# Optimization experiments

Hardware: AMD Instinct MI355X
Metric: run time of the kernel (lower is better)

The kernel has to match this reference:

```python
import jax, jax.numpy as jnp
import numpy as np

N_DRUG = 50000
N_GENE = 50000
E = 600000
D_IN = 128
D_HID = 64
D_EMB = 32


def setup_inputs() -> dict:
    key = jax.random.key(0)
    ks = jax.random.split(key, 32)
    inp = {}
    inp['x_drug'] = jax.random.normal(ks[0], (N_DRUG, D_IN), jnp.float32)
    inp['x_gene'] = jax.random.normal(ks[1], (N_GENE, D_IN), jnp.float32)
    # per-etype edge lists (src,dst)
    inp['dd_src'] = jax.random.randint(ks[2], (E,), 0, N_DRUG)
    inp['dd_dst'] = jax.random.randint(ks[3], (E,), 0, N_DRUG)
    inp['dg_src'] = jax.random.randint(ks[4], (E,), 0, N_DRUG)
    inp['dg_dst'] = jax.random.randint(ks[5], (E,), 0, N_GENE)
    inp['gd_src'] = jax.random.randint(ks[6], (E,), 0, N_GENE)
    inp['gd_dst'] = jax.random.randint(ks[7], (E,), 0, N_DRUG)
    inp['gg_src'] = jax.random.randint(ks[8], (E,), 0, N_GENE)
    inp['gg_dst'] = jax.random.randint(ks[9], (E,), 0, N_GENE)
    # layer-1 per-relation weights (in -> hidden) and per-ntype biases
    s1 = 1.0 / np.sqrt(D_IN)
    inp['W1_dd'] = jax.random.normal(ks[10], (D_IN, D_HID), jnp.float32) * s1
    inp['W1_dg'] = jax.random.normal(ks[11], (D_IN, D_HID), jnp.float32) * s1
    inp['W1_gd'] = jax.random.normal(ks[12], (D_IN, D_HID), jnp.float32) * s1
    inp['W1_gg'] = jax.random.normal(ks[13], (D_IN, D_HID), jnp.float32) * s1
    inp['b1_drug'] = jnp.zeros((D_HID,), jnp.float32)
    inp['b1_gene'] = jnp.zeros((D_HID,), jnp.float32)
    # layer-2 per-relation weights (hidden -> embed) and per-ntype biases
    s2 = 1.0 / np.sqrt(D_HID)
    inp['W2_dd'] = jax.random.normal(ks[14], (D_HID, D_EMB), jnp.float32) * s2
    inp['W2_dg'] = jax.random.normal(ks[15], (D_HID, D_EMB), jnp.float32) * s2
    inp['W2_gd'] = jax.random.normal(ks[16], (D_HID, D_EMB), jnp.float32) * s2
    inp['W2_gg'] = jax.random.normal(ks[17], (D_HID, D_EMB), jnp.float32) * s2
    inp['b2_drug'] = jnp.zeros((D_EMB,), jnp.float32)
    inp['b2_gene'] = jnp.zeros((D_EMB,), jnp.float32)
    return inp


def _rel_mean(x_src, W, src, dst, n_dst):
    # transform-then-gather (efficient when out_dim <= in_dim), segment-mean over dst
    m = (x_src @ W)[src]                                  # [E, out]
    s = jax.ops.segment_sum(m, dst, num_segments=n_dst)   # [n_dst, out]
    deg = jax.ops.segment_sum(jnp.ones((src.shape[0],), m.dtype), dst, num_segments=n_dst)
    return s / jnp.maximum(deg, 1.0)[:, None]


def _rgcn_layer(xd, xg, Wdd, Wdg, Wgd, Wgg, bd, bg,
                dd_src, dd_dst, dg_src, dg_dst, gd_src, gd_dst, gg_src, gg_dst, act):
    hd = (_rel_mean(xd, Wdd, dd_src, dd_dst, N_DRUG)
          + _rel_mean(xg, Wgd, gd_src, gd_dst, N_DRUG) + bd)
    hg = (_rel_mean(xd, Wdg, dg_src, dg_dst, N_GENE)
          + _rel_mean(xg, Wgg, gg_src, gg_dst, N_GENE) + bg)
    if act:
        hd = jax.nn.relu(hd)
        hg = jax.nn.relu(hg)
    return hd, hg


def reference(x_drug, x_gene, dd_src, dd_dst, dg_src, dg_dst, gd_src, gd_dst,
              gg_src, gg_dst, W1_dd, W1_dg, W1_gd, W1_gg, b1_drug, b1_gene,
              W2_dd, W2_dg, W2_gd, W2_gg, b2_drug, b2_gene):
    hd, hg = _rgcn_layer(x_drug, x_gene, W1_dd, W1_dg, W1_gd, W1_gg, b1_drug, b1_gene,
                         dd_src, dd_dst, dg_src, dg_dst, gd_src, gd_dst, gg_src, gg_dst, True)
    hd, hg = _rgcn_layer(hd, hg, W2_dd, W2_dg, W2_gd, W2_gg, b2_drug, b2_gene,
                         dd_src, dd_dst, dg_src, dg_dst, gd_src, gd_dst, gg_src, gg_dst, False)
    # concatenate per-ntype embeddings: rows [0:N_DRUG]=drug, [N_DRUG:]=gene
    return jnp.concatenate([hd, hg], axis=0)
```

## Files before the change

### kernel.cpp

```cpp
#include <hip/hip_runtime.h>
#include <hip/hip_bf16.h>

#define N_NODE 50000
#define NEDGE  600000
#define NRANGE 128
#define RSZ    391
#define CAPB   6144
#define CHUNK  4096
#define NBLK1  147
#define GEMM_GX 391

typedef __hip_bfloat16 bf16;
typedef __attribute__((ext_vector_type(8))) short short8;
typedef __attribute__((ext_vector_type(4))) float floatx4;

__device__ __forceinline__ short f2s(float f) {
    bf16 t = __float2bfloat16(f);
    return *(short*)&t;
}
__device__ __forceinline__ unsigned pk2(float lo, float hi) {
    return ((unsigned)(unsigned short)f2s(lo)) | (((unsigned)(unsigned short)f2s(hi)) << 16);
}
__device__ __forceinline__ void acc2(float& a, float& b, unsigned w, float m) {
    a += m * __uint_as_float(w << 16);
    b += m * __uint_as_float(w & 0xFFFF0000u);
}


__global__ __launch_bounds__(512) void k_part_gemm(
    const int* __restrict__ d0, const int* __restrict__ s0,
    const int* __restrict__ d1, const int* __restrict__ s1,
    const int* __restrict__ d2, const int* __restrict__ s2,
    const int* __restrict__ d3, const int* __restrict__ s3,
    int* __restrict__ gcur, unsigned* __restrict__ gpart,
    const float* __restrict__ X0, const float* __restrict__ X1,
    const float* __restrict__ Wa0, const float* __restrict__ Wb0,
    const float* __restrict__ Wa1, const float* __restrict__ Wb1,
    bf16* __restrict__ out0, bf16* __restrict__ out1)
{
    __shared__ union {
        struct { unsigned buf[CHUNK]; int sc[512]; int hcur[NRANGE]; int delta[NRANGE]; } p;
        short wl[4 * 8 * 512];
    } u;

    int tid = threadIdx.x;
    if (blockIdx.x < 4 * NBLK1) {
        int bid = blockIdx.x;
        int rel = bid / NBLK1;
        int c   = bid - rel * NBLK1;
        const int* dp = rel == 0 ? d0 : rel == 1 ? d1 : rel == 2 ? d2 : d3;
        const int* sp = rel == 0 ? s0 : rel == 1 ? s1 : rel == 2 ? s2 : s3;
        int e0 = c * CHUNK;
        int e1 = min(e0 + CHUNK, NEDGE);
        int cnt = e1 - e0;
        const int4* dp4 = (const int4*)(dp + e0);
        const int4* sp4 = (const int4*)(sp + e0);
        int nv = cnt >> 2;

        if (tid < NRANGE) u.p.hcur[tid] = 0;
        __syncthreads();
        for (int i = tid; i < nv; i += 512) {
            int4 d = dp4[i];
            atomicAdd(&u.p.hcur[d.x / RSZ], 1);
            atomicAdd(&u.p.hcur[d.y / RSZ], 1);
            atomicAdd(&u.p.hcur[d.z / RSZ], 1);
            atomicAdd(&u.p.hcur[d.w / RSZ], 1);
        }
        __syncthreads();
        int v = (tid < NRANGE) ? u.p.hcur[tid] : 0;
        u.p.sc[tid] = v;
        __syncthreads();
        for (int d = 1; d < NRANGE; d <<= 1) {
            int t = (tid >= d && tid < NRANGE) ? u.p.sc[tid - d] : 0;
            __syncthreads();
            if (tid < NRANGE) u.p.sc[tid] += t;
            __syncthreads();
        }
        if (tid < NRANGE) {
            int start = u.p.sc[tid] - v;
            int bg    = rel * NRANGE + tid;
            int resv  = atomicAdd(&gcur[bg], v);
            u.p.delta[tid] = bg * CAPB + resv - start;
            u.p.hcur[tid]  = start;
        }
        __syncthreads();
        for (int i = tid; i < nv; i += 512) {
            int4 d = dp4[i];
            int4 s = sp4[i];
#define PUT(dd, ss) { int b = (dd) / RSZ; int p = atomicAdd(&u.p.hcur[b], 1); \
                      u.p.buf[p] = ((unsigned)b << 25) | ((unsigned)((dd) - b * RSZ) << 16) | (unsigned)(ss); }
            PUT(d.x, s.x) PUT(d.y, s.y) PUT(d.z, s.z) PUT(d.w, s.w)
#undef PUT
        }
        __syncthreads();
        for (int i = tid * 4; i < cnt; i += 2048) {
            uint4 kb = *(const uint4*)&u.p.buf[i];
            gpart[u.p.delta[kb.x >> 25] + i + 0] = kb.x;
            gpart[u.p.delta[kb.y >> 25] + i + 1] = kb.y;
            gpart[u.p.delta[kb.z >> 25] + i + 2] = kb.z;
            gpart[u.p.delta[kb.w >> 25] + i + 3] = kb.w;
        }
    } else {
        constexpr int NB = 8, KC = 4, NH = 64;
        int bid2 = blockIdx.x - 4 * NBLK1;
        int sel  = bid2 >= GEMM_GX;
        int bx   = sel ? bid2 - GEMM_GX : bid2;
        const float* X  = sel ? X1 : X0;
        const float* Wa = sel ? Wa1 : Wa0;
        const float* Wb = sel ? Wb1 : Wb0;
        bf16*       outp = sel ? out1 : out0;

        for (int i = tid; i < KC * NB * 512; i += 512) {
            int j  = i & 7;
            int n  = (i >> 3) & 15;
            int q  = (i >> 7) & 3;
            int nb = (i >> 9) & (NB - 1);
            int kc = i >> 12;
            int k  = kc * 32 + q * 8 + j;
            int c  = nb * 16 + n;
            float w = (c < NH) ? Wa[k * NH + c] : Wb[k * NH + (c - NH)];
            u.wl[i] = f2s(w);
        }
        __syncthreads();

        int lane = tid & 63, wv = tid >> 6;
        int q = lane >> 4, lidx = lane & 15;
        int row0 = bx * 128 + wv * 16;
        int rowA = min(row0 + lidx, N_NODE - 1);

        floatx4 acc[NB];
#pragma unroll
        for (int nb = 0; nb < NB; nb++) acc[nb] = (floatx4){0.f, 0.f, 0.f, 0.f};

#pragma unroll
        for (int kc = 0; kc < KC; kc++) {
            const float* Xf = X + (size_t)rowA * 128 + kc * 32 + q * 8;
            float4 f0 = *(const float4*)Xf;
            float4 f1 = *(const float4*)(Xf + 4);
            short8 a;
            a[0] = f2s(f0.x); a[1] = f2s(f0.y); a[2] = f2s(f0.z); a[3] = f2s(f0.w);
            a[4] = f2s(f1.x); a[5] = f2s(f1.y); a[6] = f2s(f1.z); a[7] = f2s(f1.w);
#pragma unroll
            for (int nb = 0; nb < NB; nb++) {
                short8 b = *(const short8*)&u.wl[((kc * NB + nb) * 64 + lane) * 8];
                acc[nb] = __builtin_amdgcn_mfma_f32_16x16x32_bf16(a, b, acc[nb], 0, 0, 0);
            }
        }
#pragma unroll
        for (int nb = 0; nb < NB; nb++) {
#pragma unroll
            for (int r = 0; r < 4; r++) {
                int row = row0 + q * 4 + r;
                if (row < N_NODE)
                    outp[(size_t)row * 128 + nb * 16 + lidx] = __float2bfloat16(acc[nb][r]);
            }
        }
    }
}

__global__ __launch_bounds__(512) void k_csr(
    const unsigned* __restrict__ gpart, const int* __restrict__ gcnt,
    int* __restrict__ off, unsigned short* __restrict__ edges)
{
    __shared__ unsigned short stg[CAPB];
    __shared__ int cur[RSZ];
    __shared__ int sc[512];
    int bid = blockIdx.x;
    int rel = bid >> 7, r = bid & (NRANGE - 1);
    int tid = threadIdx.x;
    int range0 = r * RSZ;
    int RS = min(RSZ, N_NODE - range0);
    if (RS < 0) RS = 0;
    int count = gcnt[bid];
    const uint4* gp4 = (const uint4*)(gpart + (size_t)bid * CAPB);
    const unsigned* gp = gpart + (size_t)bid * CAPB;
    int count4 = count & ~3;

    int vb = (tid < NRANGE) ? gcnt[rel * NRANGE + tid] : 0;
    sc[tid] = vb;
    __syncthreads();
    for (int d = 1; d < NRANGE; d <<= 1) {
        int t = (tid >= d && tid < NRANGE) ? sc[tid - d] : 0;
        __syncthreads();
        if (tid < NRANGE) sc[tid] += t;
        __syncthreads();
    }
    int base = (r > 0) ? sc[r - 1] : 0;
    __syncthreads();

    for (int i = tid; i < RSZ; i += 512) cur[i] = 0;
    __syncthreads();
    for (int i = tid * 4; i < count4; i += 2048) {
        uint4 g = gp4[i >> 2];
        atomicAdd(&cur[(g.x >> 16) & 0x1FF], 1);
        atomicAdd(&cur[(g.y >> 16) & 0x1FF], 1);
        atomicAdd(&cur[(g.z >> 16) & 0x1FF], 1);
        atomicAdd(&cur[(g.w >> 16) & 0x1FF], 1);
    }
    if (tid < (count & 3))
        atomicAdd(&cur[(gp[count4 + tid] >> 16) & 0x1FF], 1);
    __syncthreads();
    int x = (tid < RSZ) ? cur[tid] : 0;
    sc[tid] = x;
    __syncthreads();
    for (int d = 1; d < 512; d <<= 1) {
        int t = (tid >= d) ? sc[tid - d] : 0;
        __syncthreads();
        sc[tid] += t;
        __syncthreads();
    }
    int excl = sc[tid] - x;
    __syncthreads();
    if (tid < RSZ) cur[tid] = excl;
    __syncthreads();
    for (int i = tid; i < RS; i += 512)
        off[rel * (N_NODE + 1) + range0 + i] = base + cur[i];
    if (r == NRANGE - 1 && tid == 0) off[rel * (N_NODE + 1) + N_NODE] = NEDGE;
    __syncthreads();
    for (int i = tid * 4; i < count4; i += 2048) {
        uint4 g = gp4[i >> 2];
#define SCAT(gg) { int p = atomicAdd(&cur[((gg) >> 16) & 0x1FF], 1); stg[p] = (unsigned short)((gg) & 0xFFFFu); }
        SCAT(g.x) SCAT(g.y) SCAT(g.z) SCAT(g.w)
#undef SCAT
    }
    if (tid < (count & 3)) {
        unsigned g = gp[count4 + tid];
        int p = atomicAdd(&cur[(g >> 16) & 0x1FF], 1);
        stg[p] = (unsigned short)(g & 0xFFFFu);
    }
    __syncthreads();
    for (int i = tid; i < count; i += 512)
        edges[(size_t)rel * NEDGE + base + i] = stg[i];
}

template <int K, int NOUT, bool AFP32>
__global__ __launch_bounds__(256) void k_gemm_pair(
    const void* __restrict__ X0, const void* __restrict__ X1,
    const float* __restrict__ Wa0, const float* __restrict__ Wb0,
    const float* __restrict__ Wa1, const float* __restrict__ Wb1,
    bf16* __restrict__ out0, bf16* __restrict__ out1, int M)
{
    constexpr int NB  = NOUT / 16;
    constexpr int KC  = K / 32;
    constexpr int NH  = NOUT / 2;
    constexpr int NBL = (NB == 8) ? 3 : 2;
    __shared__ short Wl[KC * NB * 512];

    int sel = blockIdx.y;
    const void*  X  = sel ? X1 : X0;
    const float* Wa = sel ? Wa1 : Wa0;
    const float* Wb = sel ? Wb1 : Wb0;
    bf16*        out = sel ? out1 : out0;

    int tid = threadIdx.x;
    for (int i = tid; i < KC * NB * 512; i += 256) {
        int j  = i & 7;
        int n  = (i >> 3) & 15;
        int q  = (i >> 7) & 3;
        int nb = (i >> 9) & (NB - 1);
        int kc = i >> (9 + NBL);
        int k  = kc * 32 + q * 8 + j;
        int c  = nb * 16 + n;
        float w = (c < NH) ? Wa[k * NH + c] : Wb[k * NH + (c - NH)];
        Wl[i] = f2s(w);
    }
    __syncthreads();

    int lane = tid & 63, wv = tid >> 6;
    int q = lane >> 4, lidx = lane & 15;
    int row0 = blockIdx.x * 64 + wv * 16;
    int rowA = min(row0 + lidx, M - 1);

    floatx4 acc[NB];
#pragma unroll
    for (int nb = 0; nb < NB; nb++) acc[nb] = (floatx4){0.f, 0.f, 0.f, 0.f};

#pragma unroll
    for (int kc = 0; kc < KC; kc++) {
        short8 a;
        if constexpr (AFP32) {
            const float* Xf = (const float*)X + (size_t)rowA * K + kc * 32 + q * 8;
            float4 f0 = *(const float4*)Xf;
            float4 f1 = *(const float4*)(Xf + 4);
            a[0] = f2s(f0.x); a[1] = f2s(f0.y); a[2] = f2s(f0.z); a[3] = f2s(f0.w);
            a[4] = f2s(f1.x); a[5] = f2s(f1.y); a[6] = f2s(f1.z); a[7] = f2s(f1.w);
        } else {
            a = *(const short8*)((const short*)X + (size_t)rowA * K + kc * 32 + q * 8);
        }
#pragma unroll
        for (int nb = 0; nb < NB; nb++) {
            short8 b = *(const short8*)&Wl[((kc * NB + nb) * 64 + lane) * 8];
            acc[nb] = __builtin_amdgcn_mfma_f32_16x16x32_bf16(a, b, acc[nb], 0, 0, 0);
        }
    }
#pragma unroll
    for (int nb = 0; nb < NB; nb++) {
#pragma unroll
        for (int r = 0; r < 4; r++) {
            int row = row0 + q * 4 + r;
            if (row < M)
                out[(size_t)row * NOUT + nb * 16 + lidx] = __float2bfloat16(acc[nb][r]);
        }
    }
}

template<int ROWU>
__device__ __forceinline__ void seg_run(
    int n, const unsigned short* __restrict__ ep, float sc,
    const unsigned* __restrict__ base, float* s)
{
    int nfull = n & ~3;
    for (int i = 0; i < nfull; i += 4) {
        int e0 = ep[i + 0];
        int e1 = ep[i + 1];
        int e2 = ep[i + 2];
        int e3 = ep[i + 3];
        uint4 w0 = *(const uint4*)(base + e0 * ROWU);
        uint4 w1 = *(const uint4*)(base + e1 * ROWU);
        uint4 w2 = *(const uint4*)(base + e2 * ROWU);
        uint4 w3 = *(const uint4*)(base + e3 * ROWU);
        acc2(s[0], s[1], w0.x, sc); acc2(s[2], s[3], w0.y, sc);
        acc2(s[4], s[5], w0.z, sc); acc2(s[6], s[7], w0.w, sc);
        acc2(s[0], s[1], w1.x, sc); acc2(s[2], s[3], w1.y, sc);
        acc2(s[4], s[5], w1.z, sc); acc2(s[6], s[7], w1.w, sc);
        acc2(s[0], s[1], w2.x, sc); acc2(s[2], s[3], w2.y, sc);
        acc2(s[4], s[5], w2.z, sc); acc2(s[6], s[7], w2.w, sc);
        acc2(s[0], s[1], w3.x, sc); acc2(s[2], s[3], w3.y, sc);
        acc2(s[4], s[5], w3.z, sc); acc2(s[6], s[7], w3.w, sc);
    }
    for (int i = nfull; i < n; i++) {
        int e = ep[i];
        uint4 w = *(const uint4*)(base + e * ROWU);
        acc2(s[0], s[1], w.x, sc); acc2(s[2], s[3], w.y, sc);
        acc2(s[4], s[5], w.z, sc); acc2(s[6], s[7], w.w, sc);
    }
}

__global__ __launch_bounds__(256) void k_gather64v5(
    const bf16* __restrict__ m1,
    const int* __restrict__ offA0, const unsigned short* __restrict__ eA0,
    const int* __restrict__ offB0, const unsigned short* __restrict__ eB0,
    const float* __restrict__ bias0, bf16* __restrict__ out0,
    const int* __restrict__ offA1, const unsigned short* __restrict__ eA1,
    const int* __restrict__ offB1, const unsigned short* __restrict__ eB1,
    const float* __restrict__ bias1, bf16* __restrict__ out1)
{
    int tid  = threadIdx.x;
    int gid  = blockIdx.x * 32 + (tid >> 3);
    int lidx = tid & 7;
    int half = (gid >= N_NODE);
    int wid  = gid - (half ? N_NODE : 0);
    const int* offA = half ? offA1 : offA0;
    const unsigned short* eA = half ? eA1 : eA0;
    const int* offB = half ? offB1 : offB0;
    const unsigned short* eB = half ? eB1 : eB0;
    const float* bias = half ? bias1 : bias0;
    bf16* out = half ? out1 : out0;

    const unsigned* base = (const unsigned*)m1 + (half ? 32 : 0) + lidx * 4;

    int begA = offA[wid], nA = offA[wid + 1] - begA;
    int begB = offB[wid], nB = offB[wid + 1] - begB;
    float ia = 1.f / (float)max(nA, 1);
    float ib = 1.f / (float)max(nB, 1);

    float s[8] = {0.f,0.f,0.f,0.f,0.f,0.f,0.f,0.f};
    seg_run<64>(nA, eA + begA, ia, base, s);
    seg_run<64>(nB, eB + begB, ib, base + N_NODE * 64, s);

    float h[8];
#pragma unroll
    for (int k = 0; k < 8; k++)
        h[k] = fmaxf(s[k] + bias[lidx * 8 + k], 0.f);
    uint4 v;
    v.x = pk2(h[0], h[1]); v.y = pk2(h[2], h[3]);
    v.z = pk2(h[4], h[5]); v.w = pk2(h[6], h[7]);
    *(uint4*)(out + (size_t)wid * 64 + lidx * 8) = v;
}

__global__ __launch_bounds__(256) void k_gather32v2(
    const bf16* __restrict__ m2,
    const int* __restrict__ offA0, const unsigned short* __restrict__ eA0,
    const int* __restrict__ offB0, const unsigned short* __restrict__ eB0,
    const float* __restrict__ bias0, float* __restrict__ out0,
    const int* __restrict__ offA1, const unsigned short* __restrict__ eA1,
    const int* __restrict__ offB1, const unsigned short* __restrict__ eB1,
    const float* __restrict__ bias1, float* __restrict__ out1)
{
    int tid  = threadIdx.x;
    int gid  = blockIdx.x * 64 + (tid >> 2);
    int lidx = tid & 3;
    if (gid >= 2 * N_NODE) return;
    int half = (gid >= N_NODE);
    int wid  = gid - (half ? N_NODE : 0);
    const int* offA = half ? offA1 : offA0;
    const unsigned short* eA = half ? eA1 : eA0;
    const int* offB = half ? offB1 : offB0;
    const unsigned short* eB = half ? eB1 : eB0;
    const float* bias = half ? bias1 : bias0;
    float* out = half ? out1 : out0;

    const unsigned* base = (const unsigned*)m2 + (half ? 16 : 0) + lidx * 4;

    int begA = offA[wid], nA = offA[wid + 1] - begA;
    int begB = offB[wid], nB = offB[wid + 1] - begB;
    float ia = 1.f / (float)max(nA, 1);
    float ib = 1.f / (float)max(nB, 1);

    float s[8] = {0.f,0.f,0.f,0.f,0.f,0.f,0.f,0.f};
    seg_run<32>(nA, eA + begA, ia, base, s);
    seg_run<32>(nB, eB + begB, ib, base + N_NODE * 32, s);

    float* o = out + (size_t)wid * 32 + lidx * 8;
    float4 v0, v1;
    v0.x = s[0] + bias[lidx * 8 + 0];
    v0.y = s[1] + bias[lidx * 8 + 1];
    v0.z = s[2] + bias[lidx * 8 + 2];
    v0.w = s[3] + bias[lidx * 8 + 3];
    v1.x = s[4] + bias[lidx * 8 + 4];
    v1.y = s[5] + bias[lidx * 8 + 5];
    v1.z = s[6] + bias[lidx * 8 + 6];
    v1.w = s[7] + bias[lidx * 8 + 7];
    *(float4*)o = v0;
    *(float4*)(o + 4) = v1;
}

extern "C" void kernel_launch(void* const* d_in, const int* in_sizes, int n_in,
                              void* d_out, int out_size, void* d_ws, size_t ws_size,
                              hipStream_t stream)
{
    const float* xd = (const float*)d_in[0];
    const float* xg = (const float*)d_in[1];
    const int* dd_src = (const int*)d_in[2];  const int* dd_dst = (const int*)d_in[3];
    const int* dg_src = (const int*)d_in[4];  const int* dg_dst = (const int*)d_in[5];
    const int* gd_src = (const int*)d_in[6];  const int* gd_dst = (const int*)d_in[7];
    const int* gg_src = (const int*)d_in[8];  const int* gg_dst = (const int*)d_in[9];
    const float* W1dd = (const float*)d_in[10];
    const float* W1dg = (const float*)d_in[11];
    const float* W1gd = (const float*)d_in[12];
    const float* W1gg = (const float*)d_in[13];
    const float* b1d  = (const float*)d_in[14];
    const float* b1g  = (const float*)d_in[15];
    const float* W2dd = (const float*)d_in[16];
    const float* W2dg = (const float*)d_in[17];
    const float* W2gd = (const float*)d_in[18];
    const float* W2gg = (const float*)d_in[19];
    const float* b2d  = (const float*)d_in[20];
    const float* b2g  = (const float*)d_in[21];
    float* out = (float*)d_out;

    int* gcur     = (int*)d_ws;
    int* off      = gcur + 512;
    unsigned short* edges = (unsigned short*)(off + 4 * (N_NODE + 1));
    bf16* md1     = (bf16*)(edges + (size_t)4 * NEDGE);
    bf16* mg1     = md1 + (size_t)N_NODE * 128;
    bf16* h       = mg1 + (size_t)N_NODE * 128;
    bf16* hd      = h;
    bf16* hg      = h + (size_t)N_NODE * 64;
    bf16* md2     = md1;
    bf16* mg2     = md1 + (size_t)N_NODE * 64;
    unsigned* gpart = (unsigned*)h;

    hipMemsetAsync(gcur, 0, 512 * sizeof(int), stream);
    k_part_gemm<<<4 * NBLK1 + 2 * GEMM_GX, 512, 0, stream>>>(
        dd_dst, dd_src, gd_dst, gd_src, dg_dst, dg_src, gg_dst, gg_src, gcur, gpart,
        xd, xg, W1dd, W1dg, W1gd, W1gg, md1, mg1);

    k_csr<<<512, 512, 0, stream>>>(gpart, gcur, off, edges);

    const int* off_dd = off + 0 * (N_NODE + 1);
    const int* off_gd = off + 1 * (N_NODE + 1);
    const int* off_dg = off + 2 * (N_NODE + 1);
    const int* off_gg = off + 3 * (N_NODE + 1);
    const unsigned short* e_dd = edges + (size_t)0 * NEDGE;
    const unsigned short* e_gd = edges + (size_t)1 * NEDGE;
    const unsigned short* e_dg = edges + (size_t)2 * NEDGE;
    const unsigned short* e_gg = edges + (size_t)3 * NEDGE;

    int g64_grid = (2 * N_NODE) / 32;
    int g32_grid = (2 * N_NODE + 63) / 64;
    dim3 gemm2_grid((N_NODE + 63) / 64, 2);

    k_gather64v5<<<g64_grid, 256, 0, stream>>>(
        md1,
        off_dd, e_dd, off_gd, e_gd, b1d, hd,
        off_dg, e_dg, off_gg, e_gg, b1g, hg);

    k_gemm_pair<64, 64, false><<<gemm2_grid, 256, 0, stream>>>(
        hd, hg, W2dd, W2dg, W2gd, W2gg, md2, mg2, N_NODE);

    k_gather32v2<<<g32_grid, 256, 0, stream>>>(
        md2,
        off_dd, e_dd, off_gd, e_gd, b2d, out,
        off_dg, e_dg, off_gg, e_gg, b2g, out + (size_t)N_NODE * 32);
}
```

Before: 295.9 us.

## Replace two-level partition CSR build with global histogram, offset scan, and atomic scatter

Edge-to-CSR construction no longer partitions packed keys into per-range buckets in shared memory and a global staging buffer. It now keeps per-node degree counts in global memory via atomics, computes offsets in a scan kernel, and scatters source ids with global atomics on per-node cursors. This removes the gpart staging round-trip and the local sort passes. In exchange it adds one kernel launch, a larger memset, and many contended global atomics. Edge order within each node is no longer deterministic, which can change float summation order.

```diff
diff --git a/kernel.cpp b/kernel.cpp
--- a/kernel.cpp
+++ b/kernel.cpp
@@ -2,10 +2,10 @@
 #include <hip/hip_bf16.h>
 
 #define N_NODE 50000
+#define NPAD   50048
 #define NEDGE  600000
 #define NRANGE 128
 #define RSZ    391
-#define CAPB   6144
 #define CHUNK  4096
 #define NBLK1  147
 #define GEMM_GX 391
@@ -27,19 +27,17 @@
 }
 
 
-__global__ __launch_bounds__(512) void k_part_gemm(
-    const int* __restrict__ d0, const int* __restrict__ s0,
-    const int* __restrict__ d1, const int* __restrict__ s1,
-    const int* __restrict__ d2, const int* __restrict__ s2,
-    const int* __restrict__ d3, const int* __restrict__ s3,
-    int* __restrict__ gcur, unsigned* __restrict__ gpart,
+__global__ __launch_bounds__(512) void k_hist_gemm(
+    const int* __restrict__ d0, const int* __restrict__ d1,
+    const int* __restrict__ d2, const int* __restrict__ d3,
+    int* __restrict__ rsum, int* __restrict__ cnt,
     const float* __restrict__ X0, const float* __restrict__ X1,
     const float* __restrict__ Wa0, const float* __restrict__ Wb0,
     const float* __restrict__ Wa1, const float* __restrict__ Wb1,
     bf16* __restrict__ out0, bf16* __restrict__ out1)
 {
     __shared__ union {
-        struct { unsigned buf[CHUNK]; int sc[512]; int hcur[NRANGE]; int delta[NRANGE]; } p;
+        int hcur[NRANGE];
         short wl[4 * 8 * 512];
     } u;
 
@@ -49,56 +47,25 @@
         int rel = bid / NBLK1;
         int c   = bid - rel * NBLK1;
         const int* dp = rel == 0 ? d0 : rel == 1 ? d1 : rel == 2 ? d2 : d3;
-        const int* sp = rel == 0 ? s0 : rel == 1 ? s1 : rel == 2 ? s2 : s3;
         int e0 = c * CHUNK;
         int e1 = min(e0 + CHUNK, NEDGE);
-        int cnt = e1 - e0;
+        int nv = (e1 - e0) >> 2;
         const int4* dp4 = (const int4*)(dp + e0);
-        const int4* sp4 = (const int4*)(sp + e0);
-        int nv = cnt >> 2;
-
-        if (tid < NRANGE) u.p.hcur[tid] = 0;
+        int* cntr = cnt + rel * NPAD;
+
+        if (tid < NRANGE) u.hcur[tid] = 0;
         __syncthreads();
         for (int i = tid; i < nv; i += 512) {
             int4 d = dp4[i];
-            atomicAdd(&u.p.hcur[d.x / RSZ], 1);
-            atomicAdd(&u.p.hcur[d.y / RSZ], 1);
-            atomicAdd(&u.p.hcur[d.z / RSZ], 1);
-            atomicAdd(&u.p.hcur[d.w / RSZ], 1);
-        }
-        __syncthreads();
-        int v = (tid < NRANGE) ? u.p.hcur[tid] : 0;
-        u.p.sc[tid] = v;
-        __syncthreads();
-        for (int d = 1; d < NRANGE; d <<= 1) {
-            int t = (tid >= d && tid < NRANGE) ? u.p.sc[tid - d] : 0;
-            __syncthreads();
-            if (tid < NRANGE) u.p.sc[tid] += t;
-            __syncthreads();
-        }
+            atomicAdd(&cntr[d.x], 1); atomicAdd(&u.hcur[d.x / RSZ], 1);
+            atomicAdd(&cntr[d.y], 1); atomicAdd(&u.hcur[d.y / RSZ], 1);
+            atomicAdd(&cntr[d.z], 1); atomicAdd(&u.hcur[d.z / RSZ], 1);
+            atomicAdd(&cntr[d.w], 1); atomicAdd(&u.hcur[d.w / RSZ], 1);
+        }
+        __syncthreads();
         if (tid < NRANGE) {
-            int start = u.p.sc[tid] - v;
-            int bg    = rel * NRANGE + tid;
-            int resv  = atomicAdd(&gcur[bg], v);
-            u.p.delta[tid] = bg * CAPB + resv - start;
-            u.p.hcur[tid]  = start;
-        }
-        __syncthreads();
-        for (int i = tid; i < nv; i += 512) {
-            int4 d = dp4[i];
-            int4 s = sp4[i];
-#define PUT(dd, ss) { int b = (dd) / RSZ; int p = atomicAdd(&u.p.hcur[b], 1); \
-                      u.p.buf[p] = ((unsigned)b << 25) | ((unsigned)((dd) - b * RSZ) << 16) | (unsigned)(ss); }
-            PUT(d.x, s.x) PUT(d.y, s.y) PUT(d.z, s.z) PUT(d.w, s.w)
-#undef PUT
-        }
-        __syncthreads();
-        for (int i = tid * 4; i < cnt; i += 2048) {
-            uint4 kb = *(const uint4*)&u.p.buf[i];
-            gpart[u.p.delta[kb.x >> 25] + i + 0] = kb.x;
-            gpart[u.p.delta[kb.y >> 25] + i + 1] = kb.y;
-            gpart[u.p.delta[kb.z >> 25] + i + 2] = kb.z;
-            gpart[u.p.delta[kb.w >> 25] + i + 3] = kb.w;
+            int v = u.hcur[tid];
+            if (v) atomicAdd(&rsum[rel * NRANGE + tid], v);
         }
     } else {
         constexpr int NB = 8, KC = 4, NH = 64;
@@ -158,25 +125,18 @@
     }
 }
 
-__global__ __launch_bounds__(512) void k_csr(
-    const unsigned* __restrict__ gpart, const int* __restrict__ gcnt,
-    int* __restrict__ off, unsigned short* __restrict__ edges)
-{
-    __shared__ unsigned short stg[CAPB];
-    __shared__ int cur[RSZ];
+__global__ __launch_bounds__(512) void k_off(
+    const int* __restrict__ rsum, const int* __restrict__ cnt,
+    int* __restrict__ off, int* __restrict__ cur)
+{
     __shared__ int sc[512];
     int bid = blockIdx.x;
     int rel = bid >> 7, r = bid & (NRANGE - 1);
     int tid = threadIdx.x;
     int range0 = r * RSZ;
     int RS = min(RSZ, N_NODE - range0);
-    if (RS < 0) RS = 0;
-    int count = gcnt[bid];
-    const uint4* gp4 = (const uint4*)(gpart + (size_t)bid * CAPB);
-    const unsigned* gp = gpart + (size_t)bid * CAPB;
-    int count4 = count & ~3;
-
-    int vb = (tid < NRANGE) ? gcnt[rel * NRANGE + tid] : 0;
+
+    int vb = (tid < NRANGE) ? rsum[rel * NRANGE + tid] : 0;
     sc[tid] = vb;
     __syncthreads();
     for (int d = 1; d < NRANGE; d <<= 1) {
@@ -185,22 +145,10 @@
         if (tid < NRANGE) sc[tid] += t;
         __syncthreads();
     }
-    int base = (r > 0) ? sc[r - 1] : 0;
+    int rbase = (r > 0) ? sc[r - 1] : 0;
     __syncthreads();
 
-    for (int i = tid; i < RSZ; i += 512) cur[i] = 0;
-    __syncthreads();
-    for (int i = tid * 4; i < count4; i += 2048) {
-        uint4 g = gp4[i >> 2];
-        atomicAdd(&cur[(g.x >> 16) & 0x1FF], 1);
-        atomicAdd(&cur[(g.y >> 16) & 0x1FF], 1);
-        atomicAdd(&cur[(g.z >> 16) & 0x1FF], 1);
-        atomicAdd(&cur[(g.w >> 16) & 0x1FF], 1);
-    }
-    if (tid < (count & 3))
-        atomicAdd(&cur[(gp[count4 + tid] >> 16) & 0x1FF], 1);
-    __syncthreads();
-    int x = (tid < RSZ) ? cur[tid] : 0;
+    int x = (tid < RSZ) ? cnt[rel * NPAD + range0 + tid] : 0;
     sc[tid] = x;
     __syncthreads();
     for (int d = 1; d < 512; d <<= 1) {
@@ -209,28 +157,40 @@
         sc[tid] += t;
         __syncthreads();
     }
-    int excl = sc[tid] - x;
-    __syncthreads();
-    if (tid < RSZ) cur[tid] = excl;
-    __syncthreads();
-    for (int i = tid; i < RS; i += 512)
-        off[rel * (N_NODE + 1) + range0 + i] = base + cur[i];
+    int excl = rbase + sc[tid] - x;
+    if (tid < RSZ) cur[rel * NPAD + range0 + tid] = excl;
+    if (tid < RS)  off[rel * (N_NODE + 1) + range0 + tid] = excl;
     if (r == NRANGE - 1 && tid == 0) off[rel * (N_NODE + 1) + N_NODE] = NEDGE;
-    __syncthreads();
-    for (int i = tid * 4; i < count4; i += 2048) {
-        uint4 g = gp4[i >> 2];
-#define SCAT(gg) { int p = atomicAdd(&cur[((gg) >> 16) & 0x1FF], 1); stg[p] = (unsigned short)((gg) & 0xFFFFu); }
-        SCAT(g.x) SCAT(g.y) SCAT(g.z) SCAT(g.w)
-#undef SCAT
-    }
-    if (tid < (count & 3)) {
-        unsigned g = gp[count4 + tid];
-        int p = atomicAdd(&cur[(g >> 16) & 0x1FF], 1);
-        stg[p] = (unsigned short)(g & 0xFFFFu);
-    }
-    __syncthreads();
-    for (int i = tid; i < count; i += 512)
-        edges[(size_t)rel * NEDGE + base + i] = stg[i];
+}
+
+__global__ __launch_bounds__(512) void k_scatter(
+    const int* __restrict__ d0, const int* __restrict__ s0,
+    const int* __restrict__ d1, const int* __restrict__ s1,
+    const int* __restrict__ d2, const int* __restrict__ s2,
+    const int* __restrict__ d3, const int* __restrict__ s3,
+    int* __restrict__ cur, unsigned short* __restrict__ edges)
+{
+    int bid = blockIdx.x;
+    int rel = bid / NBLK1;
+    int c   = bid - rel * NBLK1;
+    const int* dp = rel == 0 ? d0 : rel == 1 ? d1 : rel == 2 ? d2 : d3;
+    const int* sp = rel == 0 ? s0 : rel == 1 ? s1 : rel == 2 ? s2 : s3;
+    int e0 = c * CHUNK;
+    int e1 = min(e0 + CHUNK, NEDGE);
+    int nv = (e1 - e0) >> 2;
+    const int4* dp4 = (const int4*)(dp + e0);
+    const int4* sp4 = (const int4*)(sp + e0);
+    int* curr = cur + rel * NPAD;
+    unsigned short* er = edges + (size_t)rel * NEDGE;
+
+    for (int i = threadIdx.x; i < nv; i += 512) {
+        int4 d = dp4[i];
+        int4 s = sp4[i];
+        int p0 = atomicAdd(&curr[d.x], 1); er[p0] = (unsigned short)s.x;
+        int p1 = atomicAdd(&curr[d.y], 1); er[p1] = (unsigned short)s.y;
+        int p2 = atomicAdd(&curr[d.z], 1); er[p2] = (unsigned short)s.z;
+        int p3 = atomicAdd(&curr[d.w], 1); er[p3] = (unsigned short)s.w;
+    }
 }
 
 template <int K, int NOUT, bool AFP32>
@@ -449,24 +409,29 @@
     const float* b2g  = (const float*)d_in[21];
     float* out = (float*)d_out;
 
-    int* gcur     = (int*)d_ws;
-    int* off      = gcur + 512;
+    int* rsum = (int*)d_ws;
+    int* cnt  = rsum + 512;
+    int* cur  = cnt + 4 * NPAD;
+    int* off  = cur + 4 * NPAD;
     unsigned short* edges = (unsigned short*)(off + 4 * (N_NODE + 1));
-    bf16* md1     = (bf16*)(edges + (size_t)4 * NEDGE);
-    bf16* mg1     = md1 + (size_t)N_NODE * 128;
-    bf16* h       = mg1 + (size_t)N_NODE * 128;
-    bf16* hd      = h;
-    bf16* hg      = h + (size_t)N_NODE * 64;
-    bf16* md2     = md1;
-    bf16* mg2     = md1 + (size_t)N_NODE * 64;
-    unsigned* gpart = (unsigned*)h;
-
-    hipMemsetAsync(gcur, 0, 512 * sizeof(int), stream);
-    k_part_gemm<<<4 * NBLK1 + 2 * GEMM_GX, 512, 0, stream>>>(
-        dd_dst, dd_src, gd_dst, gd_src, dg_dst, dg_src, gg_dst, gg_src, gcur, gpart,
+    bf16* md1 = (bf16*)(edges + (size_t)4 * NEDGE);
+    bf16* mg1 = md1 + (size_t)N_NODE * 128;
+    bf16* h   = mg1 + (size_t)N_NODE * 128;
+    bf16* hd  = h;
+    bf16* hg  = h + (size_t)N_NODE * 64;
+    bf16* md2 = md1;
+    bf16* mg2 = md1 + (size_t)N_NODE * 64;
+
+    hipMemsetAsync(rsum, 0, (512 + 4 * NPAD) * sizeof(int), stream);
+
+    k_hist_gemm<<<4 * NBLK1 + 2 * GEMM_GX, 512, 0, stream>>>(
+        dd_dst, gd_dst, dg_dst, gg_dst, rsum, cnt,
         xd, xg, W1dd, W1dg, W1gd, W1gg, md1, mg1);
 
-    k_csr<<<512, 512, 0, stream>>>(gpart, gcur, off, edges);
+    k_off<<<512, 512, 0, stream>>>(rsum, cnt, off, cur);
+
+    k_scatter<<<4 * NBLK1, 512, 0, stream>>>(
+        dd_dst, dd_src, gd_dst, gd_src, dg_dst, dg_src, gg_dst, gg_src, cur, edges);
 
     const int* off_dd = off + 0 * (N_NODE + 1);
     const int* off_gd = off + 1 * (N_NODE + 1);
```

After: 533.3 us. 1.8x slower.

## Fuse layer-2 GEMM into layer-1 gather kernel via LDS-staged hidden tile

Applied to the files above, without the earlier changes.

The layer-1 gather kernel now keeps its 32-row hidden tile in shared memory and immediately multiplies it by the layer-2 weights with MFMA, writing the layer-2 messages directly. This removes the separate GEMM launch and the global round trip of the hidden activations. In exchange, every gather block reloads and converts all four layer-2 weight matrices into LDS and adds a barrier, which raises per-block overhead and LDS use.

```diff
diff --git a/kernel.cpp b/kernel.cpp
--- a/kernel.cpp
+++ b/kernel.cpp
@@ -231,77 +231,6 @@
     __syncthreads();
     for (int i = tid; i < count; i += 512)
         edges[(size_t)rel * NEDGE + base + i] = stg[i];
-}
-
-template <int K, int NOUT, bool AFP32>
-__global__ __launch_bounds__(256) void k_gemm_pair(
-    const void* __restrict__ X0, const void* __restrict__ X1,
-    const float* __restrict__ Wa0, const float* __restrict__ Wb0,
-    const float* __restrict__ Wa1, const float* __restrict__ Wb1,
-    bf16* __restrict__ out0, bf16* __restrict__ out1, int M)
-{
-    constexpr int NB  = NOUT / 16;
-    constexpr int KC  = K / 32;
-    constexpr int NH  = NOUT / 2;
-    constexpr int NBL = (NB == 8) ? 3 : 2;
-    __shared__ short Wl[KC * NB * 512];
-
-    int sel = blockIdx.y;
-    const void*  X  = sel ? X1 : X0;
-    const float* Wa = sel ? Wa1 : Wa0;
-    const float* Wb = sel ? Wb1 : Wb0;
-    bf16*        out = sel ? out1 : out0;
-
-    int tid = threadIdx.x;
-    for (int i = tid; i < KC * NB * 512; i += 256) {
-        int j  = i & 7;
-        int n  = (i >> 3) & 15;
-        int q  = (i >> 7) & 3;
-        int nb = (i >> 9) & (NB - 1);
-        int kc = i >> (9 + NBL);
-        int k  = kc * 32 + q * 8 + j;
-        int c  = nb * 16 + n;
-        float w = (c < NH) ? Wa[k * NH + c] : Wb[k * NH + (c - NH)];
-        Wl[i] = f2s(w);
-    }
-    __syncthreads();
-
-    int lane = tid & 63, wv = tid >> 6;
-    int q = lane >> 4, lidx = lane & 15;
-    int row0 = blockIdx.x * 64 + wv * 16;
-    int rowA = min(row0 + lidx, M - 1);
-
-    floatx4 acc[NB];
-#pragma unroll
-    for (int nb = 0; nb < NB; nb++) acc[nb] = (floatx4){0.f, 0.f, 0.f, 0.f};
-
-#pragma unroll
-    for (int kc = 0; kc < KC; kc++) {
-        short8 a;
-        if constexpr (AFP32) {
-            const float* Xf = (const float*)X + (size_t)rowA * K + kc * 32 + q * 8;
-            float4 f0 = *(const float4*)Xf;
-            float4 f1 = *(const float4*)(Xf + 4);
-            a[0] = f2s(f0.x); a[1] = f2s(f0.y); a[2] = f2s(f0.z); a[3] = f2s(f0.w);
-            a[4] = f2s(f1.x); a[5] = f2s(f1.y); a[6] = f2s(f1.z); a[7] = f2s(f1.w);
-        } else {
-            a = *(const short8*)((const short*)X + (size_t)rowA * K + kc * 32 + q * 8);
-        }
-#pragma unroll
-        for (int nb = 0; nb < NB; nb++) {
-            short8 b = *(const short8*)&Wl[((kc * NB + nb) * 64 + lane) * 8];
-            acc[nb] = __builtin_amdgcn_mfma_f32_16x16x32_bf16(a, b, acc[nb], 0, 0, 0);
-        }
-    }
-#pragma unroll
-    for (int nb = 0; nb < NB; nb++) {
-#pragma unroll
-        for (int r = 0; r < 4; r++) {
-            int row = row0 + q * 4 + r;
-            if (row < M)
-                out[(size_t)row * NOUT + nb * 16 + lidx] = __float2bfloat16(acc[nb][r]);
-        }
-    }
 }
 
 template<int ROWU>
@@ -336,16 +265,38 @@
     }
 }
 
-__global__ __launch_bounds__(256) void k_gather64v5(
+__global__ __launch_bounds__(256) void k_gather64v6(
     const bf16* __restrict__ m1,
     const int* __restrict__ offA0, const unsigned short* __restrict__ eA0,
     const int* __restrict__ offB0, const unsigned short* __restrict__ eB0,
-    const float* __restrict__ bias0, bf16* __restrict__ out0,
+    const float* __restrict__ bias0,
     const int* __restrict__ offA1, const unsigned short* __restrict__ eA1,
     const int* __restrict__ offB1, const unsigned short* __restrict__ eB1,
-    const float* __restrict__ bias1, bf16* __restrict__ out1)
-{
+    const float* __restrict__ bias1,
+    const float* __restrict__ W2dd, const float* __restrict__ W2dg,
+    const float* __restrict__ W2gd, const float* __restrict__ W2gg,
+    bf16* __restrict__ m2)
+{
+    __shared__ short wd[4096];
+    __shared__ short wg[4096];
+    __shared__ short hlds[32 * 64];
+
     int tid  = threadIdx.x;
+
+    for (int i = tid; i < 4096; i += 256) {
+        int j  = i & 7;
+        int n  = (i >> 3) & 15;
+        int q  = (i >> 7) & 3;
+        int nb = (i >> 9) & 3;
+        int kc = i >> 11;
+        int k  = kc * 32 + q * 8 + j;
+        int c  = nb * 16 + n;
+        float w0 = (c < 32) ? W2dd[k * 32 + c] : W2dg[k * 32 + (c - 32)];
+        float w1 = (c < 32) ? W2gd[k * 32 + c] : W2gg[k * 32 + (c - 32)];
+        wd[i] = f2s(w0);
+        wg[i] = f2s(w1);
+    }
+
     int gid  = blockIdx.x * 32 + (tid >> 3);
     int lidx = tid & 7;
     int half = (gid >= N_NODE);
@@ -355,7 +306,6 @@
     const int* offB = half ? offB1 : offB0;
     const unsigned short* eB = half ? eB1 : eB0;
     const float* bias = half ? bias1 : bias0;
-    bf16* out = half ? out1 : out0;
 
     const unsigned* base = (const unsigned*)m1 + (half ? 32 : 0) + lidx * 4;
 
@@ -375,7 +325,33 @@
     uint4 v;
     v.x = pk2(h[0], h[1]); v.y = pk2(h[2], h[3]);
     v.z = pk2(h[4], h[5]); v.w = pk2(h[6], h[7]);
-    *(uint4*)(out + (size_t)wid * 64 + lidx * 8) = v;
+    *(uint4*)&hlds[(tid >> 3) * 64 + lidx * 8] = v;
+    __syncthreads();
+
+    int wv = tid >> 6, lane = tid & 63;
+    int q = lane >> 4, l16 = lane & 15;
+    int rt = wv >> 1;
+    int hrow = (blockIdx.x * 32 + rt * 16) >= N_NODE;
+    const short* wsel = hrow ? wg : wd;
+    int nb0 = (wv & 1) * 2, nb1 = nb0 + 1;
+
+    floatx4 acc0 = (floatx4){0.f,0.f,0.f,0.f};
+    floatx4 acc1 = (floatx4){0.f,0.f,0.f,0.f};
+#pragma unroll
+    for (int kc = 0; kc < 2; kc++) {
+        short8 a  = *(const short8*)&hlds[(rt * 16 + l16) * 64 + kc * 32 + q * 8];
+        short8 b0 = *(const short8*)&wsel[((kc * 4 + nb0) * 64 + lane) * 8];
+        short8 b1 = *(const short8*)&wsel[((kc * 4 + nb1) * 64 + lane) * 8];
+        acc0 = __builtin_amdgcn_mfma_f32_16x16x32_bf16(a, b0, acc0, 0, 0, 0);
+        acc1 = __builtin_amdgcn_mfma_f32_16x16x32_bf16(a, b1, acc1, 0, 0, 0);
+    }
+#pragma unroll
+    for (int r = 0; r < 4; r++) {
+        int row = rt * 16 + q * 4 + r;
+        bf16* o = m2 + ((size_t)blockIdx.x * 32 + row) * 64;
+        o[nb0 * 16 + l16] = __float2bfloat16(acc0[r]);
+        o[nb1 * 16 + l16] = __float2bfloat16(acc1[r]);
+    }
 }
 
 __global__ __launch_bounds__(256) void k_gather32v2(
@@ -454,12 +430,8 @@
     unsigned short* edges = (unsigned short*)(off + 4 * (N_NODE + 1));
     bf16* md1     = (bf16*)(edges + (size_t)4 * NEDGE);
     bf16* mg1     = md1 + (size_t)N_NODE * 128;
-    bf16* h       = mg1 + (size_t)N_NODE * 128;
-    bf16* hd      = h;
-    bf16* hg      = h + (size_t)N_NODE * 64;
-    bf16* md2     = md1;
-    bf16* mg2     = md1 + (size_t)N_NODE * 64;
-    unsigned* gpart = (unsigned*)h;
+    bf16* m2      = mg1 + (size_t)N_NODE * 128;
+    unsigned* gpart = (unsigned*)m2;
 
     hipMemsetAsync(gcur, 0, 512 * sizeof(int), stream);
     k_part_gemm<<<4 * NBLK1 + 2 * GEMM_GX, 512, 0, stream>>>(
@@ -479,18 +451,15 @@
 
     int g64_grid = (2 * N_NODE) / 32;
     int g32_grid = (2 * N_NODE + 63) / 64;
-    dim3 gemm2_grid((N_NODE + 63) / 64, 2);
-
-    k_gather64v5<<<g64_grid, 256, 0, stream>>>(
+
+    k_gather64v6<<<g64_grid, 256, 0, stream>>>(
         md1,
-        off_dd, e_dd, off_gd, e_gd, b1d, hd,
-        off_dg, e_dg, off_gg, e_gg, b1g, hg);
-
-    k_gemm_pair<64, 64, false><<<gemm2_grid, 256, 0, stream>>>(
-        hd, hg, W2dd, W2dg, W2gd, W2gg, md2, mg2, N_NODE);
+        off_dd, e_dd, off_gd, e_gd, b1d,
+        off_dg, e_dg, off_gg, e_gg, b1g,
+        W2dd, W2dg, W2gd, W2gg, m2);
 
     k_gather32v2<<<g32_grid, 256, 0, stream>>>(
-        md2,
+        m2,
         off_dd, e_dd, off_gd, e_gd, b2d, out,
         off_dg, e_dg, off_gg, e_gg, b2g, out + (size_t)N_NODE * 32);
 }
```

After: 297.9 us. Within noise of the previous version (+0.7%).

## Replace shared-memory block scans with wavefront shuffle scans; coarsen partition and GEMM blocks

Applied to the files above, without the earlier changes.

Replaces the barrier-heavy shared-memory Hillis-Steele scans in the partition and CSR kernels with wave-level shuffle scans plus a small cross-wave combine. This removes many __syncthreads calls. The CSR base offset becomes a shuffle reduction over the preceding ranges. Partition chunks double to 8192 edges, which halves the block count, and each GEMM block now processes two 128-row tiles so the LDS weight staging is amortised. The trade-off is fewer blocks and more LDS per partition block, which may lower occupancy and parallelism.

```diff
diff --git a/kernel.cpp b/kernel.cpp
--- a/kernel.cpp
+++ b/kernel.cpp
@@ -6,9 +6,9 @@
 #define NRANGE 128
 #define RSZ    391
 #define CAPB   6144
-#define CHUNK  4096
-#define NBLK1  147
-#define GEMM_GX 391
+#define CHUNK  8192
+#define NBLK1  74
+#define GEMM_GB 196
 
 typedef __hip_bfloat16 bf16;
 typedef __attribute__((ext_vector_type(8))) short short8;
@@ -24,6 +24,14 @@
 __device__ __forceinline__ void acc2(float& a, float& b, unsigned w, float m) {
     a += m * __uint_as_float(w << 16);
     b += m * __uint_as_float(w & 0xFFFF0000u);
+}
+__device__ __forceinline__ int wscan(int x, int lane) {
+#pragma unroll
+    for (int d = 1; d < 64; d <<= 1) {
+        int t = __shfl_up(x, d);
+        if (lane >= d) x += t;
+    }
+    return x;
 }
 
 
@@ -39,7 +47,7 @@
     bf16* __restrict__ out0, bf16* __restrict__ out1)
 {
     __shared__ union {
-        struct { unsigned buf[CHUNK]; int sc[512]; int hcur[NRANGE]; int delta[NRANGE]; } p;
+        struct { unsigned buf[CHUNK]; int hcur[NRANGE]; int delta[NRANGE]; int wsum[2]; } p;
         short wl[4 * 8 * 512];
     } u;
 
@@ -67,17 +75,14 @@
             atomicAdd(&u.p.hcur[d.w / RSZ], 1);
         }
         __syncthreads();
+        int lane = tid & 63, wv6 = tid >> 6;
         int v = (tid < NRANGE) ? u.p.hcur[tid] : 0;
-        u.p.sc[tid] = v;
+        int inc = wscan(v, lane);
+        if (lane == 63 && wv6 < 2) u.p.wsum[wv6] = inc;
         __syncthreads();
-        for (int d = 1; d < NRANGE; d <<= 1) {
-            int t = (tid >= d && tid < NRANGE) ? u.p.sc[tid - d] : 0;
-            __syncthreads();
-            if (tid < NRANGE) u.p.sc[tid] += t;
-            __syncthreads();
-        }
         if (tid < NRANGE) {
-            int start = u.p.sc[tid] - v;
+            int incl  = inc + ((wv6 == 1) ? u.p.wsum[0] : 0);
+            int start = incl - v;
             int bg    = rel * NRANGE + tid;
             int resv  = atomicAdd(&gcur[bg], v);
             u.p.delta[tid] = bg * CAPB + resv - start;
@@ -103,8 +108,8 @@
     } else {
         constexpr int NB = 8, KC = 4, NH = 64;
         int bid2 = blockIdx.x - 4 * NBLK1;
-        int sel  = bid2 >= GEMM_GX;
-        int bx   = sel ? bid2 - GEMM_GX : bid2;
+        int sel  = bid2 >= GEMM_GB;
+        int bx   = sel ? bid2 - GEMM_GB : bid2;
         const float* X  = sel ? X1 : X0;
         const float* Wa = sel ? Wa1 : Wa0;
         const float* Wb = sel ? Wb1 : Wb0;
@@ -125,34 +130,40 @@
 
         int lane = tid & 63, wv = tid >> 6;
         int q = lane >> 4, lidx = lane & 15;
-        int row0 = bx * 128 + wv * 16;
-        int rowA = min(row0 + lidx, N_NODE - 1);
-
-        floatx4 acc[NB];
-#pragma unroll
-        for (int nb = 0; nb < NB; nb++) acc[nb] = (floatx4){0.f, 0.f, 0.f, 0.f};
-
-#pragma unroll
-        for (int kc = 0; kc < KC; kc++) {
-            const float* Xf = X + (size_t)rowA * 128 + kc * 32 + q * 8;
-            float4 f0 = *(const float4*)Xf;
-            float4 f1 = *(const float4*)(Xf + 4);
-            short8 a;
-            a[0] = f2s(f0.x); a[1] = f2s(f0.y); a[2] = f2s(f0.z); a[3] = f2s(f0.w);
-            a[4] = f2s(f1.x); a[5] = f2s(f1.y); a[6] = f2s(f1.z); a[7] = f2s(f1.w);
+
+#pragma unroll
+        for (int t = 0; t < 2; t++) {
+            int tile = bx * 2 + t;
+            if (tile * 128 >= N_NODE) break;
+            int row0 = tile * 128 + wv * 16;
+            int rowA = min(row0 + lidx, N_NODE - 1);
+
+            floatx4 acc[NB];
+#pragma unroll
+            for (int nb = 0; nb < NB; nb++) acc[nb] = (floatx4){0.f, 0.f, 0.f, 0.f};
+
+#pragma unroll
+            for (int kc = 0; kc < KC; kc++) {
+                const float* Xf = X + (size_t)rowA * 128 + kc * 32 + q * 8;
+                float4 f0 = *(const float4*)Xf;
+                float4 f1 = *(const float4*)(Xf + 4);
+                short8 a;
+                a[0] = f2s(f0.x); a[1] = f2s(f0.y); a[2] = f2s(f0.z); a[3] = f2s(f0.w);
+                a[4] = f2s(f1.x); a[5] = f2s(f1.y); a[6] = f2s(f1.z); a[7] = f2s(f1.w);
+#pragma unroll
+                for (int nb = 0; nb < NB; nb++) {
+                    short8 b = *(const short8*)&u.wl[((kc * NB + nb) * 64 + lane) * 8];
+                    acc[nb] = __builtin_amdgcn_mfma_f32_16x16x32_bf16(a, b, acc[nb], 0, 0, 0);
+                }
+            }
 #pragma unroll
             for (int nb = 0; nb < NB; nb++) {
-                short8 b = *(const short8*)&u.wl[((kc * NB + nb) * 64 + lane) * 8];
-                acc[nb] = __builtin_amdgcn_mfma_f32_16x16x32_bf16(a, b, acc[nb], 0, 0, 0);
-            }
-        }
-#pragma unroll
-        for (int nb = 0; nb < NB; nb++) {
-#pragma unroll
-            for (int r = 0; r < 4; r++) {
-                int row = row0 + q * 4 + r;
-                if (row < N_NODE)
-                    outp[(size_t)row * 128 + nb * 16 + lidx] = __float2bfloat16(acc[nb][r]);
+#pragma unroll
+                for (int r = 0; r < 4; r++) {
+                    int row = row0 + q * 4 + r;
+                    if (row < N_NODE)
+                        outp[(size_t)row * 128 + nb * 16 + lidx] = __float2bfloat16(acc[nb][r]);
+                }
             }
         }
     }
@@ -164,10 +175,11 @@
 {
     __shared__ unsigned short stg[CAPB];
     __shared__ int cur[RSZ];
-    __shared__ int sc[512];
+    __shared__ int wsum[8];
     int bid = blockIdx.x;
     int rel = bid >> 7, r = bid & (NRANGE - 1);
     int tid = threadIdx.x;
+    int lane = tid & 63, wv = tid >> 6;
     int range0 = r * RSZ;
     int RS = min(RSZ, N_NODE - range0);
     if (RS < 0) RS = 0;
@@ -176,20 +188,14 @@
     const unsigned* gp = gpart + (size_t)bid * CAPB;
     int count4 = count & ~3;
 
-    int vb = (tid < NRANGE) ? gcnt[rel * NRANGE + tid] : 0;
-    sc[tid] = vb;
-    __syncthreads();
-    for (int d = 1; d < NRANGE; d <<= 1) {
-        int t = (tid >= d && tid < NRANGE) ? sc[tid - d] : 0;
-        __syncthreads();
-        if (tid < NRANGE) sc[tid] += t;
-        __syncthreads();
-    }
-    int base = (r > 0) ? sc[r - 1] : 0;
-    __syncthreads();
-
+    int vb = (tid < r) ? gcnt[rel * NRANGE + tid] : 0;
+#pragma unroll
+    for (int d = 32; d; d >>= 1) vb += __shfl_xor(vb, d);
+    if (lane == 0 && wv < 2) wsum[wv] = vb;
     for (int i = tid; i < RSZ; i += 512) cur[i] = 0;
     __syncthreads();
+    int base = wsum[0] + wsum[1];
+
     for (int i = tid * 4; i < count4; i += 2048) {
         uint4 g = gp4[i >> 2];
         atomicAdd(&cur[(g.x >> 16) & 0x1FF], 1);
@@ -200,23 +206,22 @@
     if (tid < (count & 3))
         atomicAdd(&cur[(gp[count4 + tid] >> 16) & 0x1FF], 1);
     __syncthreads();
+
     int x = (tid < RSZ) ? cur[tid] : 0;
-    sc[tid] = x;
+    int inc = wscan(x, lane);
+    if (lane == 63) wsum[wv] = inc;
     __syncthreads();
-    for (int d = 1; d < 512; d <<= 1) {
-        int t = (tid >= d) ? sc[tid - d] : 0;
-        __syncthreads();
-        sc[tid] += t;
-        __syncthreads();
-    }
-    int excl = sc[tid] - x;
-    __syncthreads();
+    int pre = 0;
+#pragma unroll
+    for (int w = 0; w < 7; w++) pre += (w < wv) ? wsum[w] : 0;
+    int excl = inc + pre - x;
     if (tid < RSZ) cur[tid] = excl;
     __syncthreads();
-    for (int i = tid; i < RS; i += 512)
-        off[rel * (N_NODE + 1) + range0 + i] = base + cur[i];
+
+    if (tid < RS)
+        off[rel * (N_NODE + 1) + range0 + tid] = base + cur[tid];
     if (r == NRANGE - 1 && tid == 0) off[rel * (N_NODE + 1) + N_NODE] = NEDGE;
-    __syncthreads();
+
     for (int i = tid * 4; i < count4; i += 2048) {
         uint4 g = gp4[i >> 2];
 #define SCAT(gg) { int p = atomicAdd(&cur[((gg) >> 16) & 0x1FF], 1); stg[p] = (unsigned short)((gg) & 0xFFFFu); }
@@ -462,7 +467,7 @@
     unsigned* gpart = (unsigned*)h;
 
     hipMemsetAsync(gcur, 0, 512 * sizeof(int), stream);
-    k_part_gemm<<<4 * NBLK1 + 2 * GEMM_GX, 512, 0, stream>>>(
+    k_part_gemm<<<4 * NBLK1 + 2 * GEMM_GB, 512, 0, stream>>>(
         dd_dst, dd_src, gd_dst, gd_src, dg_dst, dg_src, gg_dst, gg_src, gcur, gpart,
         xd, xg, W1dd, W1dg, W1gd, W1gg, md1, mg1);
 
```

New measurement: 289.7 us (median of 2 runs). 1.02x faster.
